# Kernel optimization log

Measured on AMD Instinct MI355X. Metric: run time of the kernel, lower is better.

Reference implementation:

```python
import jax, jax.numpy as jnp
import numpy as np

N, F, H, K = 8192, 128, 128, 16
E = N * 32


def _mlp(f, w1, b1, w2, b2, w3, b3):
    h = jax.nn.relu(f @ w1 + b1)
    h = jax.nn.relu(h @ w2 + b2)
    return h @ w3 + b3


def _edge_conv(x, w1, b1, w2, b2, w3, b3, k):
    # dynamic kNN in feature space (includes self like torch_cluster.knn with x==y)
    sn = jnp.sum(x * x, axis=1)
    d = sn[:, None] + sn[None, :] - 2.0 * (x @ x.T)  # [N,N] squared dists
    idx = jax.lax.top_k(-d, k)[1]                    # [N,k] nearest neighbors
    xj = x[idx]                                      # [N,k,H]
    xi = jnp.broadcast_to(x[:, None, :], xj.shape)
    f = jnp.concatenate([xi, xj - xi], axis=-1)      # [N,k,2H]
    return jnp.max(_mlp(f, w1, b1, w2, b2, w3, b3), axis=1)  # max aggregation


def _gcn(x, w, b, src, dst, norm, n):
    h = x @ w
    out = jax.ops.segment_sum(norm[:, None] * h[src], dst, num_segments=n)
    return out + b


def _forward(x, edge_index, edge_weight,
             wg1, bg1, wg2, bg2, wg3, bg3,
             e1w1, e1b1, e1w2, e1b2, e1w3, e1b3,
             e2w1, e2b1, e2w2, e2b2, e2w3, e2b3,
             e3w1, e3b1, e3w2, e3b2, e3w3, e3b3):
    n = x.shape[0]
    loop = jnp.arange(n)
    src = jnp.concatenate([edge_index[0], loop])  # source j
    dst = jnp.concatenate([edge_index[1], loop])  # target i
    ew = jnp.concatenate([edge_weight, jnp.ones((n,), x.dtype)])  # self-loop weight 1
    deg = jax.ops.segment_sum(ew, dst, num_segments=n)
    dis = jnp.where(deg > 0, jax.lax.rsqrt(jnp.maximum(deg, 1e-12)), 0.0)
    norm = dis[src] * ew * dis[dst]

    n1 = jnp.tanh(_gcn(x, wg1, bg1, src, dst, norm, n))   # dropout is identity at eval
    e1 = _edge_conv(n1, e1w1, e1b1, e1w2, e1b2, e1w3, e1b3, K)
    e1_n1 = jnp.linalg.norm(e1 + n1, axis=1, keepdims=True)  # [N,1]

    n2 = jnp.tanh(_gcn(n1, wg2, bg2, src, dst, norm, n))
    e2 = _edge_conv(n2, e2w1, e2b1, e2w2, e2b2, e2w3, e2b3, K)
    e2_n2 = e2 + n2

    n3 = jnp.tanh(_gcn(n2, wg3, bg3, src, dst, norm, n))
    e3 = _edge_conv(n3, e3w1, e3b1, e3w2, e3b2, e3w3, e3b3, K)
    e3_n3 = e3 + n3

    x2 = e1_n1 * e2_n2 * e3_n3
    return jax.nn.log_softmax(x2, axis=1)


def setup_inputs() -> dict:
    key = jax.random.key(0)
    ks = jax.random.split(key, 32)
    inp = {
        'x': jax.random.normal(ks[0], (N, F), dtype=jnp.float32),
        'edge_index': jax.random.randint(ks[1], (2, E), 0, N, dtype=jnp.int64) if jax.config.jax_enable_x64 else jax.random.randint(ks[1], (2, E), 0, N).astype(jnp.int32),
        'edge_weight': jax.random.uniform(ks[2], (E,), dtype=jnp.float32),
    }
    s = 0.05
    gcn_in = [F, H, H]
    for i in range(3):
        inp[f'wg{i+1}'] = jax.random.normal(ks[3 + i], (gcn_in[i], H), dtype=jnp.float32) * s
        inp[f'bg{i+1}'] = jnp.zeros((H,), jnp.float32)
    dims = [(2 * H, 64), (64, H), (H, H)]
    kk = 6
    for c in range(1, 4):
        for j, (di, do) in enumerate(dims):
            inp[f'e{c}w{j+1}'] = jax.random.normal(ks[kk], (di, do), dtype=jnp.float32) * s
            inp[f'e{c}b{j+1}'] = jnp.zeros((do,), jnp.float32)
            kk += 1
    return inp


def reference(x, edge_index, edge_weight,
              wg1, bg1, wg2, bg2, wg3, bg3,
              e1w1, e1b1, e1w2, e1b2, e1w3, e1b3,
              e2w1, e2b1, e2w2, e2b2, e2w3, e2b3,
              e3w1, e3b1, e3w2, e3b2, e3w3, e3b3):
    return _forward(x, edge_index, edge_weight,
                    wg1, bg1, wg2, bg2, wg3, bg3,
                    e1w1, e1b1, e1w2, e1b2, e1w3, e1b3,
                    e2w1, e2b1, e2w2, e2b2, e2w3, e2b3,
                    e3w1, e3b1, e3w2, e3b2, e3w3, e3b3)
```

## Files before the change

kernel.cpp:

```cpp
#include <hip/hip_runtime.h>
#include <math.h>

#define N_ 8192
#define H_ 128
#define E_ 262144
#define K_ 16
#define SLABJ 1024
#define CHUNKJ 512

typedef __attribute__((ext_vector_type(8))) short bshort8;
typedef __attribute__((ext_vector_type(16))) float f32x16;
typedef unsigned long long u64;

__global__ void k_deg_init(float* deg) {
  int i = blockIdx.x * 256 + threadIdx.x;
  deg[i] = 1.0f;
}

__global__ void k_deg_scatter(const int* __restrict__ ei, const float* __restrict__ ew,
                              float* deg) {
  int e = blockIdx.x * 256 + threadIdx.x;
  atomicAdd(&deg[ei[E_ + e]], ew[e]);
}

__global__ void k_dis(float* deg) {
  int i = blockIdx.x * 256 + threadIdx.x;
  deg[i] = rsqrtf(deg[i]);
}

__global__ void k_hist(const int* __restrict__ ei, int* hist) {
  int e = blockIdx.x * 256 + threadIdx.x;
  atomicAdd(&hist[ei[E_ + e]], 1);
}

__global__ void k_scan(int* hist, int* rowptr) {
  __shared__ int part[256];
  __shared__ int partx[257];
  int t = threadIdx.x;
  int base = t * 32;
  int loc[32];
  int s = 0;
#pragma unroll
  for (int i = 0; i < 32; ++i) { loc[i] = s; s += hist[base + i]; }
  part[t] = s;
  __syncthreads();
  if (t == 0) {
    int r = 0;
    for (int i = 0; i < 256; ++i) { partx[i] = r; r += part[i]; }
    partx[256] = r;
  }
  __syncthreads();
  int b = partx[t];
#pragma unroll
  for (int i = 0; i < 32; ++i) {
    rowptr[base + i] = b + loc[i];
    hist[base + i] = b + loc[i];
  }
  if (t == 0) rowptr[N_] = partx[256];
}

__global__ void k_edgebuild(const int* __restrict__ ei, const float* __restrict__ ew,
                            const float* __restrict__ dis, int* cursor,
                            int* __restrict__ srcS, float* __restrict__ normS) {
  int e = blockIdx.x * 256 + threadIdx.x;
  int s = ei[e], d = ei[E_ + e];
  int pos = atomicAdd(&cursor[d], 1);
  srcS[pos] = s;
  normS[pos] = dis[s] * ew[e] * dis[d];
}

__device__ __forceinline__ unsigned short f2bf_rne(float x) {
  unsigned u = __builtin_bit_cast(unsigned, x);
  unsigned r = ((u >> 16) & 1u) + 0x7fffu;
  return (unsigned short)((u + r) >> 16);
}
__device__ __forceinline__ float bf2f(unsigned short b) {
  unsigned u = ((unsigned)b) << 16;
  return __builtin_bit_cast(float, u);
}

__global__ void k_wprepG(const float* __restrict__ w, int mode,
                         bshort8* __restrict__ outH, bshort8* __restrict__ outL) {
  int id = blockIdx.x * 256 + threadIdx.x;
  int lane = id & 63, ks = (id >> 6) & 7, nt = id >> 9;
  int n = nt * 32 + (lane & 31);
  int k0 = ks * 16 + (lane >> 5) * 8;
  bshort8 h, l;
#pragma unroll
  for (int i = 0; i < 8; ++i) {
    int k = k0 + i;
    float v;
    if (mode == 0) v = w[k * 128 + n];
    else v = (n < 64) ? (w[k * 64 + n] - w[(128 + k) * 64 + n])
                      : w[(128 + k) * 64 + (n - 64)];
    unsigned short hb = f2bf_rne(v);
    h[i] = (short)hb;
    l[i] = (short)f2bf_rne(v - bf2f(hb));
  }
  outH[id] = h;
  outL[id] = l;
}

__global__ __launch_bounds__(256, 3) void k_gemmM(const float* __restrict__ A,
                                                  const bshort8* __restrict__ wfH,
                                                  const bshort8* __restrict__ wfL,
                                                  float* __restrict__ C) {
  __shared__ short aHs[32 * 132], aLs[32 * 132];
  int t = threadIdx.x;
  int r0 = blockIdx.x * 32;
  int w = t >> 6, lane = t & 63, q = lane & 31, half = lane >> 5;

  {
    int r = t >> 3;
    int kc = (t & 7) * 16;
    const float* p = A + (r0 + r) * 128 + kc;
#pragma unroll
    for (int e4 = 0; e4 < 4; ++e4) {
      float4 v = *(const float4*)(p + e4 * 4);
      float vals[4] = {v.x, v.y, v.z, v.w};
      unsigned short hs[4], ls[4];
#pragma unroll
      for (int i = 0; i < 4; ++i) {
        hs[i] = f2bf_rne(vals[i]);
        ls[i] = f2bf_rne(vals[i] - bf2f(hs[i]));
      }
      int off = r * 132 + kc + e4 * 4;
      *(u64*)&aHs[off] = ((u64)hs[0]) | ((u64)hs[1] << 16) | ((u64)hs[2] << 32) | ((u64)hs[3] << 48);
      *(u64*)&aLs[off] = ((u64)ls[0]) | ((u64)ls[1] << 16) | ((u64)ls[2] << 32) | ((u64)ls[3] << 48);
    }
  }
  bshort8 bH[8], bL[8];
#pragma unroll
  for (int ks = 0; ks < 8; ++ks) {
    bH[ks] = wfH[(w * 8 + ks) * 64 + lane];
    bL[ks] = wfL[(w * 8 + ks) * 64 + lane];
  }
  __syncthreads();

  f32x16 accP, accQ;
#pragma unroll
  for (int r = 0; r < 16; ++r) { accP[r] = 0.f; accQ[r] = 0.f; }
#pragma unroll
  for (int ks = 0; ks < 8; ++ks) {
    int off = q * 132 + ks * 16 + half * 8;
    union { bshort8 v; u64 u[2]; } aH, aL;
    aH.u[0] = *(const u64*)&aHs[off];
    aH.u[1] = *(const u64*)&aHs[off + 4];
    aL.u[0] = *(const u64*)&aLs[off];
    aL.u[1] = *(const u64*)&aLs[off + 4];
    accQ = __builtin_amdgcn_mfma_f32_32x32x16_bf16(aL.v, bH[ks], accQ, 0, 0, 0);
    accQ = __builtin_amdgcn_mfma_f32_32x32x16_bf16(aH.v, bL[ks], accQ, 0, 0, 0);
    accP = __builtin_amdgcn_mfma_f32_32x32x16_bf16(aH.v, bH[ks], accP, 0, 0, 0);
  }
#pragma unroll
  for (int reg = 0; reg < 16; ++reg) {
    int row = (reg & 3) + 8 * (reg >> 2) + 4 * half;
    C[(r0 + row) * 128 + w * 32 + q] = accP[reg] + accQ[reg];
  }
}

__global__ __launch_bounds__(256) void k_gcn_agg(const float* __restrict__ h,
                                                 const float* __restrict__ dis,
                                                 const int* __restrict__ rowptr,
                                                 const int* __restrict__ srcS,
                                                 const float* __restrict__ normS,
                                                 const float* __restrict__ bg,
                                                 float* __restrict__ n_out,
                                                 float* __restrict__ sn) {
  __shared__ float part[4];
  int t = threadIdx.x;
  int i = blockIdx.x * 2 + (t >> 7);
  int c = t & 127;
  float di = dis[i];
  float a0 = di * di * h[i * 128 + c], a1 = 0.f, a2 = 0.f, a3 = 0.f;
  int e0 = rowptr[i], e1 = rowptr[i + 1];
  int e = e0;
  for (; e + 4 <= e1; e += 4) {
    int s0 = srcS[e], s1 = srcS[e + 1], s2 = srcS[e + 2], s3 = srcS[e + 3];
    float w0 = normS[e], w1 = normS[e + 1], w2 = normS[e + 2], w3 = normS[e + 3];
    a0 += w0 * h[s0 * 128 + c];
    a1 += w1 * h[s1 * 128 + c];
    a2 += w2 * h[s2 * 128 + c];
    a3 += w3 * h[s3 * 128 + c];
  }
  for (; e < e1; ++e) a0 += normS[e] * h[srcS[e] * 128 + c];
  float v = tanhf(a0 + a1 + a2 + a3 + bg[c]);
  n_out[i * 128 + c] = v;
  float vv = v * v;
#pragma unroll
  for (int off = 32; off; off >>= 1) vv += __shfl_down(vv, off, 64);
  if ((t & 63) == 0) part[t >> 6] = vv;
  __syncthreads();
  if ((t & 127) == 0) sn[i] = part[t >> 6] + part[(t >> 6) + 1];
}

__global__ void k_fragprep(const float* __restrict__ src, bshort8* __restrict__ hiA,
                           bshort8* __restrict__ loA) {
  int t = blockIdx.x * 256 + threadIdx.x;
  int j = t >> 4, slot = t & 15;
  const float* p = src + j * 128 + slot * 8;
  float4 f0 = *(const float4*)p;
  float4 f1 = *(const float4*)(p + 4);
  float f[8] = {f0.x, f0.y, f0.z, f0.w, f1.x, f1.y, f1.z, f1.w};
  bshort8 h, l;
#pragma unroll
  for (int i = 0; i < 8; ++i) {
    unsigned short hb = f2bf_rne(f[i]);
    h[i] = (short)hb;
    l[i] = (short)f2bf_rne(f[i] - bf2f(hb));
  }
  int ks = slot >> 1, half = slot & 1;
  int dst = ((j >> 5) * 8 + ks) * 64 + half * 32 + (j & 31);
  hiA[dst] = h;
  loA[dst] = l;
}

__device__ __forceinline__ u64 packkey(float d, int j) {
  unsigned m = __builtin_bit_cast(unsigned, d);
  m = (m & 0x80000000u) ? ~m : (m | 0x80000000u);
  return (((u64)m) << 32) | (unsigned)j;
}

__device__ __forceinline__ void ins8(u64* tk, u64 x) {
  bool c[8];
#pragma unroll
  for (int s = 0; s < 8; ++s) c[s] = x < tk[s];
#pragma unroll
  for (int s = 7; s >= 1; --s) tk[s] = c[s - 1] ? tk[s - 1] : (c[s] ? x : tk[s]);
  tk[0] = c[0] ? x : tk[0];
}

__device__ __forceinline__ void ins16(u64* tk, u64 x) {
  bool c[16];
#pragma unroll
  for (int s = 0; s < 16; ++s) c[s] = x < tk[s];
#pragma unroll
  for (int s = 15; s >= 1; --s) tk[s] = c[s - 1] ? tk[s - 1] : (c[s] ? x : tk[s]);
  tk[0] = c[0] ? x : tk[0];
}

__global__ __launch_bounds__(256, 3) void k_knnA(const bshort8* __restrict__ fragHi,
                                                 const bshort8* __restrict__ fragLo,
                                                 const float* __restrict__ sn,
                                                 u64* __restrict__ candA) {
  __shared__ float snS[CHUNKJ];
  __shared__ u64 mbuf[32 * 65];
  int t = threadIdx.x;
  int qtile = blockIdx.x, chunk = blockIdx.y;
  int wave = t >> 6, lane = t & 63;
  int q = lane & 31, half = lane >> 5;

  snS[t] = sn[chunk * CHUNKJ + t];
  snS[t + 256] = sn[chunk * CHUNKJ + t + 256];

  bshort8 bHi[8], bLo[8];
#pragma unroll
  for (int ks = 0; ks < 8; ++ks) {
    int o = (qtile * 8 + ks) * 64 + lane;
    bHi[ks] = fragHi[o];
    bLo[ks] = fragLo[o];
  }
  __syncthreads();

  u64 tk[8];
#pragma unroll
  for (int s = 0; s < 8; ++s) tk[s] = ~0ULL;

  for (int ti = 0; ti < 4; ++ti) {
    int jt = chunk * 16 + wave * 4 + ti;
    f32x16 accP, accQ;
#pragma unroll
    for (int r = 0; r < 16; ++r) { accP[r] = 0.f; accQ[r] = 0.f; }
    {
      bshort8 aH[4], aL[4];
#pragma unroll
      for (int k4 = 0; k4 < 4; ++k4) {
        int o = (jt * 8 + k4) * 64 + lane;
        aH[k4] = fragHi[o];
        aL[k4] = fragLo[o];
      }
#pragma unroll
      for (int k4 = 0; k4 < 4; ++k4) {
        accQ = __builtin_amdgcn_mfma_f32_32x32x16_bf16(aL[k4], bHi[k4], accQ, 0, 0, 0);
        accQ = __builtin_amdgcn_mfma_f32_32x32x16_bf16(aH[k4], bLo[k4], accQ, 0, 0, 0);
        accP = __builtin_amdgcn_mfma_f32_32x32x16_bf16(aH[k4], bHi[k4], accP, 0, 0, 0);
      }
    }
    {
      bshort8 aH[4], aL[4];
#pragma unroll
      for (int k4 = 0; k4 < 4; ++k4) {
        int o = (jt * 8 + 4 + k4) * 64 + lane;
        aH[k4] = fragHi[o];
        aL[k4] = fragLo[o];
      }
#pragma unroll
      for (int k4 = 0; k4 < 4; ++k4) {
        accQ = __builtin_amdgcn_mfma_f32_32x32x16_bf16(aL[k4], bHi[4 + k4], accQ, 0, 0, 0);
        accQ = __builtin_amdgcn_mfma_f32_32x32x16_bf16(aH[k4], bLo[4 + k4], accQ, 0, 0, 0);
        accP = __builtin_amdgcn_mfma_f32_32x32x16_bf16(aH[k4], bHi[4 + k4], accP, 0, 0, 0);
      }
    }

    int jbase = (wave * 4 + ti) * 32;
#pragma unroll
    for (int rp = 0; rp < 8; ++rp) {
      int r0 = rp * 2;
      int row0 = (r0 & 3) + 8 * (r0 >> 2) + 4 * half;
      float d0 = snS[jbase + row0] - 2.0f * (accP[r0] + accQ[r0]);
      float d1 = snS[jbase + row0 + 1] - 2.0f * (accP[r0 + 1] + accQ[r0 + 1]);
      u64 k0 = packkey(d0, chunk * CHUNKJ + jbase + row0);
      u64 k1 = packkey(d1, chunk * CHUNKJ + jbase + row0 + 1);
      u64 km = k0 < k1 ? k0 : k1;
      if (km < tk[7]) {
        if (k0 < tk[7]) ins8(tk, k0);
        if (k1 < tk[7]) ins8(tk, k1);
      }
    }
  }

  int g = wave * 2 + half;
  __syncthreads();
#pragma unroll
  for (int s = 0; s < 8; ++s) mbuf[q * 65 + g * 8 + s] = tk[s];
  __syncthreads();
  if (t < 32) {
    int qq = qtile * 32 + t;
    int base = t * 65;
    int h0 = 0, h1 = 0, h2 = 0, h3 = 0, h4 = 0, h5 = 0, h6 = 0, h7 = 0;
    for (int step = 0; step < 16; ++step) {
      u64 best = (h0 < 8) ? mbuf[base + h0] : ~0ULL;
      int bg = 0;
      u64 b;
      b = (h1 < 8) ? mbuf[base + 8 + h1] : ~0ULL;  if (b < best) { best = b; bg = 1; }
      b = (h2 < 8) ? mbuf[base + 16 + h2] : ~0ULL; if (b < best) { best = b; bg = 2; }
      b = (h3 < 8) ? mbuf[base + 24 + h3] : ~0ULL; if (b < best) { best = b; bg = 3; }
      b = (h4 < 8) ? mbuf[base + 32 + h4] : ~0ULL; if (b < best) { best = b; bg = 4; }
      b = (h5 < 8) ? mbuf[base + 40 + h5] : ~0ULL; if (b < best) { best = b; bg = 5; }
      b = (h6 < 8) ? mbuf[base + 48 + h6] : ~0ULL; if (b < best) { best = b; bg = 6; }
      b = (h7 < 8) ? mbuf[base + 56 + h7] : ~0ULL; if (b < best) { best = b; bg = 7; }
      candA[(chunk * 16 + step) * N_ + qq] = best;
      h0 += (bg == 0); h1 += (bg == 1); h2 += (bg == 2); h3 += (bg == 3);
      h4 += (bg == 4); h5 += (bg == 5); h6 += (bg == 6); h7 += (bg == 7);
    }
  }
}

__global__ __launch_bounds__(64) void k_tauseed(const u64* __restrict__ candA,
                                                u64* __restrict__ accept,
                                                int* __restrict__ cursor,
                                                u64* __restrict__ tauKey) {
  int q = blockIdx.x * 64 + threadIdx.x;
  int h0 = 0, h1 = 0, h2 = 0, h3 = 0;
  u64 best = 0;
  for (int step = 0; step < 16; ++step) {
    best = candA[h0 * N_ + q];
    int bg = 0;
    u64 b;
    b = candA[(16 + h1) * N_ + q]; if (b < best) { best = b; bg = 1; }
    b = candA[(32 + h2) * N_ + q]; if (b < best) { best = b; bg = 2; }
    b = candA[(48 + h3) * N_ + q]; if (b < best) { best = b; bg = 3; }
    accept[step * N_ + q] = best;
    h0 += (bg == 0); h1 += (bg == 1); h2 += (bg == 2); h3 += (bg == 3);
  }
  tauKey[q] = best;
  cursor[q] = 16;
}

__global__ __launch_bounds__(256, 3) void k_knnB(const bshort8* __restrict__ fragHi,
                                                 const bshort8* __restrict__ fragLo,
                                                 const float* __restrict__ sn,
                                                 const u64* __restrict__ tauKey,
                                                 int* __restrict__ cursor,
                                                 u64* __restrict__ accept,
                                                 u64* __restrict__ accExt) {
  __shared__ float snS[SLABJ];
  int t = threadIdx.x;
  int qtile = blockIdx.x, slab = blockIdx.y + 2;
  int wave = t >> 6, lane = t & 63;
  int q = lane & 31, half = lane >> 5;
  int qg = qtile * 32 + q;

#pragma unroll
  for (int p = 0; p < 4; ++p) snS[t + 256 * p] = sn[slab * SLABJ + t + 256 * p];

  bshort8 bHi[8], bLo[8];
#pragma unroll
  for (int ks = 0; ks < 8; ++ks) {
    int o = (qtile * 8 + ks) * 64 + lane;
    bHi[ks] = fragHi[o];
    bLo[ks] = fragLo[o];
  }
  u64 tau = tauKey[qg];
  __syncthreads();

  u64 buf[6];
  int cnt = 0;

  for (int ti = 0; ti < 8; ++ti) {
    int jt = slab * 32 + wave * 8 + ti;
    f32x16 accP, accQ;
#pragma unroll
    for (int r = 0; r < 16; ++r) { accP[r] = 0.f; accQ[r] = 0.f; }
    {
      bshort8 aH[4], aL[4];
#pragma unroll
      for (int k4 = 0; k4 < 4; ++k4) {
        int o = (jt * 8 + k4) * 64 + lane;
        aH[k4] = fragHi[o];
        aL[k4] = fragLo[o];
      }
#pragma unroll
      for (int k4 = 0; k4 < 4; ++k4) {
        accQ = __builtin_amdgcn_mfma_f32_32x32x16_bf16(aL[k4], bHi[k4], accQ, 0, 0, 0);
        accQ = __builtin_amdgcn_mfma_f32_32x32x16_bf16(aH[k4], bLo[k4], accQ, 0, 0, 0);
        accP = __builtin_amdgcn_mfma_f32_32x32x16_bf16(aH[k4], bHi[k4], accP, 0, 0, 0);
      }
    }
    {
      bshort8 aH[4], aL[4];
#pragma unroll
      for (int k4 = 0; k4 < 4; ++k4) {
        int o = (jt * 8 + 4 + k4) * 64 + lane;
        aH[k4] = fragHi[o];
        aL[k4] = fragLo[o];
      }
#pragma unroll
      for (int k4 = 0; k4 < 4; ++k4) {
        accQ = __builtin_amdgcn_mfma_f32_32x32x16_bf16(aL[k4], bHi[4 + k4], accQ, 0, 0, 0);
        accQ = __builtin_amdgcn_mfma_f32_32x32x16_bf16(aH[k4], bLo[4 + k4], accQ, 0, 0, 0);
        accP = __builtin_amdgcn_mfma_f32_32x32x16_bf16(aH[k4], bHi[4 + k4], accP, 0, 0, 0);
      }
    }

    int jbase = (wave * 8 + ti) * 32;
#pragma unroll
    for (int rp = 0; rp < 8; ++rp) {
      int r0 = rp * 2;
      int row0 = (r0 & 3) + 8 * (r0 >> 2) + 4 * half;
      float d0 = snS[jbase + row0] - 2.0f * (accP[r0] + accQ[r0]);
      float d1 = snS[jbase + row0 + 1] - 2.0f * (accP[r0 + 1] + accQ[r0 + 1]);
      u64 k0 = packkey(d0, slab * SLABJ + jbase + row0);
      u64 k1 = packkey(d1, slab * SLABJ + jbase + row0 + 1);
      if (k0 <= tau) {
        if (cnt < 6) {
#pragma unroll
          for (int s = 0; s < 6; ++s)
            if (s == cnt) buf[s] = k0;
          ++cnt;
        } else {
          int pos = atomicAdd(&cursor[qg], 1);
          if (pos < 128) accept[(size_t)pos * N_ + qg] = k0;
          else if (pos < 192) accExt[(size_t)(pos - 128) * N_ + qg] = k0;
        }
      }
      if (k1 <= tau) {
        if (cnt < 6) {
#pragma unroll
          for (int s = 0; s < 6; ++s)
            if (s == cnt) buf[s] = k1;
          ++cnt;
        } else {
          int pos = atomicAdd(&cursor[qg], 1);
          if (pos < 128) accept[(size_t)pos * N_ + qg] = k1;
          else if (pos < 192) accExt[(size_t)(pos - 128) * N_ + qg] = k1;
        }
      }
    }
  }

  if (cnt > 0) {
    int pos = atomicAdd(&cursor[qg], cnt);
#pragma unroll
    for (int s = 0; s < 6; ++s) {
      if (s < cnt) {
        int slot = pos + s;
        if (slot < 128) accept[(size_t)slot * N_ + qg] = buf[s];
        else if (slot < 192) accExt[(size_t)(slot - 128) * N_ + qg] = buf[s];
      }
    }
  }
}

__global__ __launch_bounds__(256) void k_select(const u64* __restrict__ accept,
                                                const u64* __restrict__ accExt,
                                                const int* __restrict__ cursor,
                                                int* __restrict__ idxo) {
  __shared__ u64 mb[64 * 65];
  int t = threadIdx.x;
  int ql = t >> 2;
  int j = t & 3;
  int q = blockIdx.x * 64 + ql;
  int c = cursor[q];
  if (c > 192) c = 192;
  u64 tk[16];
#pragma unroll
  for (int s = 0; s < 16; ++s) tk[s] = ~0ULL;
  for (int i = j; i < c; i += 4) {
    u64 x = (i < 128) ? accept[(size_t)i * N_ + q] : accExt[(size_t)(i - 128) * N_ + q];
    if (x < tk[15]) ins16(tk, x);
  }
#pragma unroll
  for (int s = 0; s < 16; ++s) mb[ql * 65 + j * 16 + s] = tk[s];
  __syncthreads();
  if (t < 64) {
    int qq = blockIdx.x * 64 + t;
    int base = t * 65;
    int h0 = 0, h1 = 0, h2 = 0, h3 = 0;
    for (int step = 0; step < 16; ++step) {
      u64 best = mb[base + h0];
      int bg = 0;
      u64 b;
      b = mb[base + 16 + h1]; if (b < best) { best = b; bg = 1; }
      b = mb[base + 32 + h2]; if (b < best) { best = b; bg = 2; }
      b = mb[base + 48 + h3]; if (b < best) { best = b; bg = 3; }
      idxo[qq * 16 + step] = (int)(unsigned)(best & 0xffffffffULL);
      h0 += (bg == 0); h1 += (bg == 1); h2 += (bg == 2); h3 += (bg == 3);
    }
  }
}

__global__ void k_wprep(const float* __restrict__ w2, const float* __restrict__ w3,
                        bshort8* __restrict__ w2fH, bshort8* __restrict__ w2fL,
                        bshort8* __restrict__ w3fH, bshort8* __restrict__ w3fL) {
  int id = blockIdx.x * 256 + threadIdx.x;
  const float* src;
  bshort8 *dH, *dL;
  int n, k0, slot;
  if (id < 1024) {
    int lane = id & 63, ks = (id >> 6) & 3, nt = id >> 8;
    n = nt * 32 + (lane & 31);
    k0 = ks * 16 + (lane >> 5) * 8;
    src = w2; dH = w2fH; dL = w2fL; slot = id;
  } else {
    int id2 = id - 1024;
    int lane = id2 & 63, ks = (id2 >> 6) & 7, nt = id2 >> 9;
    n = nt * 32 + (lane & 31);
    k0 = ks * 16 + (lane >> 5) * 8;
    src = w3; dH = w3fH; dL = w3fL; slot = id2;
  }
  bshort8 h, l;
#pragma unroll
  for (int i = 0; i < 8; ++i) {
    float v = src[(k0 + i) * 128 + n];
    unsigned short hb = f2bf_rne(v);
    h[i] = (short)hb;
    l[i] = (short)f2bf_rne(v - bf2f(hb));
  }
  dH[slot] = h;
  dL[slot] = l;
}

__global__ __launch_bounds__(256, 3) void k_mlpM(
    const float* __restrict__ ab, const int* __restrict__ idx,
    const bshort8* __restrict__ w2fH, const bshort8* __restrict__ w2fL,
    const bshort8* __restrict__ w3fH, const bshort8* __restrict__ w3fL,
    const float* __restrict__ b1g, const float* __restrict__ b2g,
    const float* __restrict__ b3g, const float* __restrict__ nadd,
    float* __restrict__ eout) {
  __shared__ short h1H[64 * 68], h1L[64 * 68];
  __shared__ short h2H[64 * 132], h2L[64 * 132];
  int t = threadIdx.x;
  int n0 = blockIdx.x * 4;
  int w = t >> 6, lane = t & 63, q = lane & 31, half = lane >> 5;

  {
    int r = t >> 2;
    int kc = (t & 3) * 16;
    int node = n0 + (r >> 4);
    int jn = idx[node * 16 + (r & 15)];
    const float* pa = ab + node * 128 + kc;
    const float* pb = ab + jn * 128 + 64 + kc;
    const float* p1 = b1g + kc;
#pragma unroll
    for (int e4 = 0; e4 < 4; ++e4) {
      float4 va = *(const float4*)(pa + e4 * 4);
      float4 vb = *(const float4*)(pb + e4 * 4);
      float4 v1 = *(const float4*)(p1 + e4 * 4);
      float vals[4] = {va.x + vb.x + v1.x, va.y + vb.y + v1.y,
                       va.z + vb.z + v1.z, va.w + vb.w + v1.w};
      unsigned short hs[4], ls[4];
#pragma unroll
      for (int i = 0; i < 4; ++i) {
        float v = fmaxf(vals[i], 0.f);
        hs[i] = f2bf_rne(v);
        ls[i] = f2bf_rne(v - bf2f(hs[i]));
      }
      int off = r * 68 + kc + e4 * 4;
      *(u64*)&h1H[off] = ((u64)hs[0]) | ((u64)hs[1] << 16) | ((u64)hs[2] << 32) | ((u64)hs[3] << 48);
      *(u64*)&h1L[off] = ((u64)ls[0]) | ((u64)ls[1] << 16) | ((u64)ls[2] << 32) | ((u64)ls[3] << 48);
    }
  }

  bshort8 c2H[4], c2L[4];
#pragma unroll
  for (int ks = 0; ks < 4; ++ks) {
    c2H[ks] = w2fH[(w * 4 + ks) * 64 + lane];
    c2L[ks] = w2fL[(w * 4 + ks) * 64 + lane];
  }
  bshort8 c3H[8], c3L[8];
#pragma unroll
  for (int ks = 0; ks < 8; ++ks) {
    c3H[ks] = w3fH[(w * 8 + ks) * 64 + lane];
    c3L[ks] = w3fL[(w * 8 + ks) * 64 + lane];
  }
  float bias2 = b2g[w * 32 + q];
  float bias3 = b3g[w * 32 + q];
  __syncthreads();

#pragma unroll
  for (int rt = 0; rt < 2; ++rt) {
    f32x16 acc;
#pragma unroll
    for (int r = 0; r < 16; ++r) acc[r] = 0.f;
#pragma unroll
    for (int ks = 0; ks < 4; ++ks) {
      int off = (rt * 32 + q) * 68 + ks * 16 + half * 8;
      union { bshort8 v; u64 u[2]; } aH, aL;
      aH.u[0] = *(const u64*)&h1H[off];
      aH.u[1] = *(const u64*)&h1H[off + 4];
      aL.u[0] = *(const u64*)&h1L[off];
      aL.u[1] = *(const u64*)&h1L[off + 4];
      acc = __builtin_amdgcn_mfma_f32_32x32x16_bf16(aL.v, c2H[ks], acc, 0, 0, 0);
      acc = __builtin_amdgcn_mfma_f32_32x32x16_bf16(aH.v, c2L[ks], acc, 0, 0, 0);
      acc = __builtin_amdgcn_mfma_f32_32x32x16_bf16(aH.v, c2H[ks], acc, 0, 0, 0);
    }
#pragma unroll
    for (int reg = 0; reg < 16; ++reg) {
      int row = rt * 32 + (reg & 3) + 8 * (reg >> 2) + 4 * half;
      float v = fmaxf(acc[reg] + bias2, 0.f);
      unsigned short hb = f2bf_rne(v);
      h2H[row * 132 + w * 32 + q] = (short)hb;
      h2L[row * 132 + w * 32 + q] = (short)f2bf_rne(v - bf2f(hb));
    }
  }
  __syncthreads();

#pragma unroll
  for (int rt = 0; rt < 2; ++rt) {
    f32x16 acc;
#pragma unroll
    for (int r = 0; r < 16; ++r) acc[r] = 0.f;
#pragma unroll
    for (int ks = 0; ks < 8; ++ks) {
      int off = (rt * 32 + q) * 132 + ks * 16 + half * 8;
      union { bshort8 v; u64 u[2]; } aH, aL;
      aH.u[0] = *(const u64*)&h2H[off];
      aH.u[1] = *(const u64*)&h2H[off + 4];
      aL.u[0] = *(const u64*)&h2L[off];
      aL.u[1] = *(const u64*)&h2L[off + 4];
      acc = __builtin_amdgcn_mfma_f32_32x32x16_bf16(aL.v, c3H[ks], acc, 0, 0, 0);
      acc = __builtin_amdgcn_mfma_f32_32x32x16_bf16(aH.v, c3L[ks], acc, 0, 0, 0);
      acc = __builtin_amdgcn_mfma_f32_32x32x16_bf16(aH.v, c3H[ks], acc, 0, 0, 0);
    }
    float mA = -INFINITY, mB = -INFINITY;
#pragma unroll
    for (int reg = 0; reg < 8; ++reg) mA = fmaxf(mA, acc[reg]);
#pragma unroll
    for (int reg = 8; reg < 16; ++reg) mB = fmaxf(mB, acc[reg]);
    mA = fmaxf(mA, __shfl_xor(mA, 32, 64));
    mB = fmaxf(mB, __shfl_xor(mB, 32, 64));
    int col = w * 32 + q;
    int nodeA = n0 + rt * 2, nodeB = n0 + rt * 2 + 1;
    if (half == 0) {
      float v = mA + bias3;
      if (nadd) v += nadd[nodeA * 128 + col];
      eout[nodeA * 128 + col] = v;
    } else {
      float v = mB + bias3;
      if (nadd) v += nadd[nodeB * 128 + col];
      eout[nodeB * 128 + col] = v;
    }
  }
}

__global__ void k_e1n1(const float* __restrict__ e1, const float* __restrict__ n1,
                       float* s1) {
  int t = threadIdx.x;
  int node = blockIdx.x * 4 + (t >> 6);
  int lane = t & 63;
  float v0 = e1[node * 128 + lane] + n1[node * 128 + lane];
  float v1 = e1[node * 128 + 64 + lane] + n1[node * 128 + 64 + lane];
  float ss = v0 * v0 + v1 * v1;
#pragma unroll
  for (int off = 32; off; off >>= 1) ss += __shfl_down(ss, off, 64);
  if (lane == 0) s1[node] = sqrtf(ss);
}

__global__ void k_final(const float* __restrict__ s1, const float* __restrict__ e2n2,
                        const float* __restrict__ e3n3, float* __restrict__ out) {
  int t = threadIdx.x;
  int node = blockIdx.x * 4 + (t >> 6);
  int lane = t & 63;
  float s = s1[node];
  float z0 = s * e2n2[node * 128 + lane] * e3n3[node * 128 + lane];
  float z1 = s * e2n2[node * 128 + 64 + lane] * e3n3[node * 128 + 64 + lane];
  float m = fmaxf(z0, z1);
#pragma unroll
  for (int off = 32; off; off >>= 1) m = fmaxf(m, __shfl_xor(m, off, 64));
  float ex = expf(z0 - m) + expf(z1 - m);
#pragma unroll
  for (int off = 32; off; off >>= 1) ex += __shfl_xor(ex, off, 64);
  float lse = m + logf(ex);
  out[node * 128 + lane] = z0 - lse;
  out[node * 128 + 64 + lane] = z1 - lse;
}

extern "C" void kernel_launch(void* const* d_in, const int* in_sizes, int n_in,
                              void* d_out, int out_size, void* d_ws, size_t ws_size,
                              hipStream_t stream) {
  (void)in_sizes; (void)n_in; (void)out_size;
  const float* x  = (const float*)d_in[0];
  const int* ei   = (const int*)d_in[1];
  const float* ew = (const float*)d_in[2];
  const float* wg[3] = {(const float*)d_in[3], (const float*)d_in[5], (const float*)d_in[7]};
  const float* bg[3] = {(const float*)d_in[4], (const float*)d_in[6], (const float*)d_in[8]};
  const float* ew1[3] = {(const float*)d_in[9],  (const float*)d_in[15], (const float*)d_in[21]};
  const float* eb1[3] = {(const float*)d_in[10], (const float*)d_in[16], (const float*)d_in[22]};
  const float* ew2[3] = {(const float*)d_in[11], (const float*)d_in[17], (const float*)d_in[23]};
  const float* eb2[3] = {(const float*)d_in[12], (const float*)d_in[18], (const float*)d_in[24]};
  const float* ew3[3] = {(const float*)d_in[13], (const float*)d_in[19], (const float*)d_in[25]};
  const float* eb3[3] = {(const float*)d_in[14], (const float*)d_in[20], (const float*)d_in[26]};

  size_t small = (size_t)(22 * N_ + (N_ + 256) + N_ + 2 * E_);
  size_t need = (small + 65536 + (size_t)7 * N_ * H_) * sizeof(float);
  if (ws_size < need) return;

  float* ws  = (float*)d_ws;
  float* dis = ws;
  float* sn  = ws + N_;
  float* S1  = ws + 2 * N_;
  int* idx   = (int*)(ws + 3 * N_);
  u64* tauKey = (u64*)(ws + 19 * N_);
  int* cursor = (int*)(ws + 21 * N_);
  int* rowptr = (int*)(ws + 22 * N_);
  int* hist   = rowptr + N_ + 256;
  int* srcS   = hist + N_;
  float* normS = (float*)(srcS + E_);
  float* wfrag = normS + E_;
  bshort8* wgfH = (bshort8*)wfrag;
  bshort8* wgfL = wgfH + 4096;
  bshort8* w1fH = wgfL + 4096;
  bshort8* w1fL = w1fH + 4096;
  float* h   = wfrag + 65536;
  float* n1  = h + N_ * H_;
  float* n2  = n1 + N_ * H_;
  float* n3  = n2 + N_ * H_;
  float* E2  = n3 + N_ * H_;
  float* E1  = E2 + N_ * H_;
  float* ab  = E1 + N_ * H_;

  bshort8* fragHi = (bshort8*)h;
  bshort8* fragLo = (bshort8*)(h + N_ * H_ / 2);
  u64* candA  = (u64*)ab;
  u64* accept = (u64*)E1;
  bshort8* w2fH = (bshort8*)h;
  bshort8* w2fL = w2fH + 1024;
  bshort8* w3fH = w2fL + 1024;
  bshort8* w3fL = w3fH + 2048;

  float* nl[3] = {n1, n2, n3};
  float* spare[3] = {n2, n1, n2};
  float* nadd[3] = {nullptr, n2, n3};

  k_deg_init<<<N_ / 256, 256, 0, stream>>>(dis);
  k_deg_scatter<<<E_ / 256, 256, 0, stream>>>(ei, ew, dis);
  k_dis<<<N_ / 256, 256, 0, stream>>>(dis);
  hipMemsetAsync(hist, 0, N_ * sizeof(int), stream);
  k_hist<<<E_ / 256, 256, 0, stream>>>(ei, hist);
  k_scan<<<1, 256, 0, stream>>>(hist, rowptr);
  k_edgebuild<<<E_ / 256, 256, 0, stream>>>(ei, ew, dis, hist, srcS, normS);

  for (int l = 0; l < 3; ++l) {
    const float* inp = (l == 0) ? x : nl[l - 1];
    k_wprepG<<<8, 256, 0, stream>>>(wg[l], 0, wgfH, wgfL);
    k_gemmM<<<256, 256, 0, stream>>>(inp, wgfH, wgfL, h);
    k_gcn_agg<<<N_ / 2, 256, 0, stream>>>(h, dis, rowptr, srcS, normS, bg[l], nl[l], sn);
    k_fragprep<<<N_ * 16 / 256, 256, 0, stream>>>(nl[l], fragHi, fragLo);
    k_knnA<<<dim3(N_ / 32, 4), 256, 0, stream>>>(fragHi, fragLo, sn, candA);
    k_tauseed<<<N_ / 64, 64, 0, stream>>>(candA, accept, cursor, tauKey);
    k_knnB<<<dim3(N_ / 32, 6), 256, 0, stream>>>(fragHi, fragLo, sn, tauKey, cursor,
                                                 accept, (u64*)spare[l]);
    k_select<<<N_ / 64, 256, 0, stream>>>(accept, (u64*)spare[l], cursor, idx);
    k_wprepG<<<8, 256, 0, stream>>>(ew1[l], 1, w1fH, w1fL);
    k_wprep<<<12, 256, 0, stream>>>(ew2[l], ew3[l], w2fH, w2fL, w3fH, w3fL);
    k_gemmM<<<256, 256, 0, stream>>>(nl[l], w1fH, w1fL, ab);
    float* etgt = (l == 1) ? E2 : E1;
    k_mlpM<<<N_ / 4, 256, 0, stream>>>(ab, idx, w2fH, w2fL, w3fH, w3fL,
                                       eb1[l], eb2[l], eb3[l], nadd[l], etgt);
    if (l == 0) k_e1n1<<<N_ / 4, 256, 0, stream>>>(E1, n1, S1);
  }
  k_final<<<N_ / 4, 256, 0, stream>>>(S1, E2, E1, (float*)d_out);
}
```

Before: 842.1 us.

## Batch weight prep, reuse kNN fragments for MLP GEMM, restructure kNN candidate merge

All twelve weight matrices are now converted to bf16 hi/lo fragments in one launch before the layer loop, replacing three prep kernels per layer. The first edge-MLP GEMM reads the already-built kNN fragment buffers instead of re-splitting the fp32 activations. The kNN first pass now processes 1024-column slabs over 2 chunks and writes per-wave top-8 lists straight to global memory, and the in-block shared-memory merge moves into a wider tau-seed kernel. knnB also compares float distances against a precomputed float threshold instead of building packed keys first. The costs are more global traffic for the unmerged candidates, lower grid parallelism in knnA, and a possible change in tie handling at the threshold.

```diff
diff --git a/kernel.cpp b/kernel.cpp
--- a/kernel.cpp
+++ b/kernel.cpp
@@ -6,7 +6,6 @@
 #define E_ 262144
 #define K_ 16
 #define SLABJ 1024
-#define CHUNKJ 512
 
 typedef __attribute__((ext_vector_type(8))) short bshort8;
 typedef __attribute__((ext_vector_type(16))) float f32x16;
@@ -79,26 +78,45 @@
   return __builtin_bit_cast(float, u);
 }
 
-__global__ void k_wprepG(const float* __restrict__ w, int mode,
-                         bshort8* __restrict__ outH, bshort8* __restrict__ outL) {
+struct WP { const float* p[12]; };
+
+__global__ void k_wprepAll(WP wp, bshort8* __restrict__ wAll) {
   int id = blockIdx.x * 256 + threadIdx.x;
-  int lane = id & 63, ks = (id >> 6) & 7, nt = id >> 9;
-  int n = nt * 32 + (lane & 31);
-  int k0 = ks * 16 + (lane >> 5) * 8;
+  int layer = id / 7168;
+  int r = id - layer * 7168;
+  bshort8* base = wAll + layer * 14336;
+  const float* src;
+  bshort8 *dH, *dL;
+  int slot, kind;
+  if (r < 2048)      { kind = 0; slot = r;        src = wp.p[layer*4+0]; dH = base;         dL = base + 2048; }
+  else if (r < 4096) { kind = 1; slot = r - 2048; src = wp.p[layer*4+1]; dH = base + 4096;  dL = base + 6144; }
+  else if (r < 5120) { kind = 2; slot = r - 4096; src = wp.p[layer*4+2]; dH = base + 8192;  dL = base + 9216; }
+  else               { kind = 3; slot = r - 5120; src = wp.p[layer*4+3]; dH = base + 10240; dL = base + 12288; }
+  int lane = slot & 63;
+  int n, k0;
+  if (kind == 2) {
+    int ks = (slot >> 6) & 3, nt = slot >> 8;
+    n = nt * 32 + (lane & 31);
+    k0 = ks * 16 + (lane >> 5) * 8;
+  } else {
+    int ks = (slot >> 6) & 7, nt = slot >> 9;
+    n = nt * 32 + (lane & 31);
+    k0 = ks * 16 + (lane >> 5) * 8;
+  }
   bshort8 h, l;
 #pragma unroll
   for (int i = 0; i < 8; ++i) {
     int k = k0 + i;
     float v;
-    if (mode == 0) v = w[k * 128 + n];
-    else v = (n < 64) ? (w[k * 64 + n] - w[(128 + k) * 64 + n])
-                      : w[(128 + k) * 64 + (n - 64)];
+    if (kind == 1) v = (n < 64) ? (src[k * 64 + n] - src[(128 + k) * 64 + n])
+                                : src[(128 + k) * 64 + (n - 64)];
+    else v = src[k * 128 + n];
     unsigned short hb = f2bf_rne(v);
     h[i] = (short)hb;
     l[i] = (short)f2bf_rne(v - bf2f(hb));
   }
-  outH[id] = h;
-  outL[id] = l;
+  dH[slot] = h;
+  dL[slot] = l;
 }
 
 __global__ __launch_bounds__(256, 3) void k_gemmM(const float* __restrict__ A,
@@ -156,6 +174,38 @@
   for (int reg = 0; reg < 16; ++reg) {
     int row = (reg & 3) + 8 * (reg >> 2) + 4 * half;
     C[(r0 + row) * 128 + w * 32 + q] = accP[reg] + accQ[reg];
+  }
+}
+
+__global__ void k_gemmMF(const bshort8* __restrict__ fAH, const bshort8* __restrict__ fAL,
+                         const bshort8* __restrict__ wfH, const bshort8* __restrict__ wfL,
+                         float* __restrict__ C) {
+  int t = threadIdx.x;
+  int rt = blockIdx.x >> 1;
+  int w = (blockIdx.x & 1) * 2 + (t >> 6);
+  int lane = t & 63, q = lane & 31, half = lane >> 5;
+
+  bshort8 bH[8], bL[8], aH[8], aL[8];
+#pragma unroll
+  for (int ks = 0; ks < 8; ++ks) {
+    bH[ks] = wfH[(w * 8 + ks) * 64 + lane];
+    bL[ks] = wfL[(w * 8 + ks) * 64 + lane];
+    aH[ks] = fAH[(rt * 8 + ks) * 64 + lane];
+    aL[ks] = fAL[(rt * 8 + ks) * 64 + lane];
+  }
+  f32x16 accP, accQ;
+#pragma unroll
+  for (int r = 0; r < 16; ++r) { accP[r] = 0.f; accQ[r] = 0.f; }
+#pragma unroll
+  for (int ks = 0; ks < 8; ++ks) {
+    accQ = __builtin_amdgcn_mfma_f32_32x32x16_bf16(aL[ks], bH[ks], accQ, 0, 0, 0);
+    accQ = __builtin_amdgcn_mfma_f32_32x32x16_bf16(aH[ks], bL[ks], accQ, 0, 0, 0);
+    accP = __builtin_amdgcn_mfma_f32_32x32x16_bf16(aH[ks], bH[ks], accP, 0, 0, 0);
+  }
+#pragma unroll
+  for (int reg = 0; reg < 16; ++reg) {
+    int row = (reg & 3) + 8 * (reg >> 2) + 4 * half;
+    C[(rt * 32 + row) * 128 + w * 32 + q] = accP[reg] + accQ[reg];
   }
 }
 
@@ -221,6 +271,12 @@
   return (((u64)m) << 32) | (unsigned)j;
 }
 
+__device__ __forceinline__ float unpackd(u64 key) {
+  unsigned m = (unsigned)(key >> 32);
+  unsigned u = (m & 0x80000000u) ? (m & 0x7fffffffu) : ~m;
+  return __builtin_bit_cast(float, u);
+}
+
 __device__ __forceinline__ void ins8(u64* tk, u64 x) {
   bool c[8];
 #pragma unroll
@@ -242,16 +298,15 @@
 __global__ __launch_bounds__(256, 3) void k_knnA(const bshort8* __restrict__ fragHi,
                                                  const bshort8* __restrict__ fragLo,
                                                  const float* __restrict__ sn,
-                                                 u64* __restrict__ candA) {
-  __shared__ float snS[CHUNKJ];
-  __shared__ u64 mbuf[32 * 65];
+                                                 u64* __restrict__ candR) {
+  __shared__ float snS[SLABJ];
   int t = threadIdx.x;
   int qtile = blockIdx.x, chunk = blockIdx.y;
   int wave = t >> 6, lane = t & 63;
   int q = lane & 31, half = lane >> 5;
 
-  snS[t] = sn[chunk * CHUNKJ + t];
-  snS[t + 256] = sn[chunk * CHUNKJ + t + 256];
+#pragma unroll
+  for (int p = 0; p < 4; ++p) snS[t + 256 * p] = sn[chunk * SLABJ + t + 256 * p];
 
   bshort8 bHi[8], bLo[8];
 #pragma unroll
@@ -266,8 +321,8 @@
 #pragma unroll
   for (int s = 0; s < 8; ++s) tk[s] = ~0ULL;
 
-  for (int ti = 0; ti < 4; ++ti) {
-    int jt = chunk * 16 + wave * 4 + ti;
+  for (int ti = 0; ti < 8; ++ti) {
+    int jt = chunk * 32 + wave * 8 + ti;
     f32x16 accP, accQ;
 #pragma unroll
     for (int r = 0; r < 16; ++r) { accP[r] = 0.f; accQ[r] = 0.f; }
@@ -302,15 +357,15 @@
       }
     }
 
-    int jbase = (wave * 4 + ti) * 32;
+    int jbase = (wave * 8 + ti) * 32;
 #pragma unroll
     for (int rp = 0; rp < 8; ++rp) {
       int r0 = rp * 2;
       int row0 = (r0 & 3) + 8 * (r0 >> 2) + 4 * half;
       float d0 = snS[jbase + row0] - 2.0f * (accP[r0] + accQ[r0]);
       float d1 = snS[jbase + row0 + 1] - 2.0f * (accP[r0 + 1] + accQ[r0 + 1]);
-      u64 k0 = packkey(d0, chunk * CHUNKJ + jbase + row0);
-      u64 k1 = packkey(d1, chunk * CHUNKJ + jbase + row0 + 1);
+      u64 k0 = packkey(d0, chunk * SLABJ + jbase + row0);
+      u64 k1 = packkey(d1, chunk * SLABJ + jbase + row0 + 1);
       u64 km = k0 < k1 ? k0 : k1;
       if (km < tk[7]) {
         if (k0 < tk[7]) ins8(tk, k0);
@@ -320,57 +375,64 @@
   }
 
   int g = wave * 2 + half;
-  __syncthreads();
-#pragma unroll
-  for (int s = 0; s < 8; ++s) mbuf[q * 65 + g * 8 + s] = tk[s];
-  __syncthreads();
-  if (t < 32) {
-    int qq = qtile * 32 + t;
+#pragma unroll
+  for (int s = 0; s < 8; ++s)
+    candR[(size_t)(chunk * 64 + g * 8 + s) * N_ + qtile * 32 + q] = tk[s];
+}
+
+__global__ __launch_bounds__(256) void k_tauseedX(const u64* __restrict__ candR,
+                                                  u64* __restrict__ accept,
+                                                  int* __restrict__ cursor,
+                                                  u64* __restrict__ tauKey,
+                                                  float* __restrict__ tauD) {
+  __shared__ u64 mb[64 * 65];
+  int t = threadIdx.x;
+  int ql = t >> 2, j = t & 3;
+  int q = blockIdx.x * 64 + ql;
+
+  int rb[4];
+#pragma unroll
+  for (int k = 0; k < 4; ++k) {
+    int L = 4 * j + k;
+    rb[k] = (L >> 3) * 64 + (L & 7) * 8;
+  }
+  int h0 = 0, h1 = 0, h2 = 0, h3 = 0;
+  for (int step = 0; step < 16; ++step) {
+    u64 best = (h0 < 8) ? candR[(size_t)(rb[0] + h0) * N_ + q] : ~0ULL;
+    int bg = 0;
+    u64 b;
+    b = (h1 < 8) ? candR[(size_t)(rb[1] + h1) * N_ + q] : ~0ULL; if (b < best) { best = b; bg = 1; }
+    b = (h2 < 8) ? candR[(size_t)(rb[2] + h2) * N_ + q] : ~0ULL; if (b < best) { best = b; bg = 2; }
+    b = (h3 < 8) ? candR[(size_t)(rb[3] + h3) * N_ + q] : ~0ULL; if (b < best) { best = b; bg = 3; }
+    mb[ql * 65 + j * 16 + step] = best;
+    h0 += (bg == 0); h1 += (bg == 1); h2 += (bg == 2); h3 += (bg == 3);
+  }
+  __syncthreads();
+  if (t < 64) {
+    int qq = blockIdx.x * 64 + t;
     int base = t * 65;
-    int h0 = 0, h1 = 0, h2 = 0, h3 = 0, h4 = 0, h5 = 0, h6 = 0, h7 = 0;
+    int g0 = 0, g1 = 0, g2 = 0, g3 = 0;
+    u64 best = 0;
     for (int step = 0; step < 16; ++step) {
-      u64 best = (h0 < 8) ? mbuf[base + h0] : ~0ULL;
+      best = mb[base + g0];
       int bg = 0;
       u64 b;
-      b = (h1 < 8) ? mbuf[base + 8 + h1] : ~0ULL;  if (b < best) { best = b; bg = 1; }
-      b = (h2 < 8) ? mbuf[base + 16 + h2] : ~0ULL; if (b < best) { best = b; bg = 2; }
-      b = (h3 < 8) ? mbuf[base + 24 + h3] : ~0ULL; if (b < best) { best = b; bg = 3; }
-      b = (h4 < 8) ? mbuf[base + 32 + h4] : ~0ULL; if (b < best) { best = b; bg = 4; }
-      b = (h5 < 8) ? mbuf[base + 40 + h5] : ~0ULL; if (b < best) { best = b; bg = 5; }
-      b = (h6 < 8) ? mbuf[base + 48 + h6] : ~0ULL; if (b < best) { best = b; bg = 6; }
-      b = (h7 < 8) ? mbuf[base + 56 + h7] : ~0ULL; if (b < best) { best = b; bg = 7; }
-      candA[(chunk * 16 + step) * N_ + qq] = best;
-      h0 += (bg == 0); h1 += (bg == 1); h2 += (bg == 2); h3 += (bg == 3);
-      h4 += (bg == 4); h5 += (bg == 5); h6 += (bg == 6); h7 += (bg == 7);
-    }
-  }
-}
-
-__global__ __launch_bounds__(64) void k_tauseed(const u64* __restrict__ candA,
-                                                u64* __restrict__ accept,
-                                                int* __restrict__ cursor,
-                                                u64* __restrict__ tauKey) {
-  int q = blockIdx.x * 64 + threadIdx.x;
-  int h0 = 0, h1 = 0, h2 = 0, h3 = 0;
-  u64 best = 0;
-  for (int step = 0; step < 16; ++step) {
-    best = candA[h0 * N_ + q];
-    int bg = 0;
-    u64 b;
-    b = candA[(16 + h1) * N_ + q]; if (b < best) { best = b; bg = 1; }
-    b = candA[(32 + h2) * N_ + q]; if (b < best) { best = b; bg = 2; }
-    b = candA[(48 + h3) * N_ + q]; if (b < best) { best = b; bg = 3; }
-    accept[step * N_ + q] = best;
-    h0 += (bg == 0); h1 += (bg == 1); h2 += (bg == 2); h3 += (bg == 3);
-  }
-  tauKey[q] = best;
-  cursor[q] = 16;
+      b = mb[base + 16 + g1]; if (b < best) { best = b; bg = 1; }
+      b = mb[base + 32 + g2]; if (b < best) { best = b; bg = 2; }
+      b = mb[base + 48 + g3]; if (b < best) { best = b; bg = 3; }
+      accept[(size_t)step * N_ + qq] = best;
+      g0 += (bg == 0); g1 += (bg == 1); g2 += (bg == 2); g3 += (bg == 3);
+    }
+    tauKey[qq] = best;
+    tauD[qq] = unpackd(best);
+    cursor[qq] = 16;
+  }
 }
 
 __global__ __launch_bounds__(256, 3) void k_knnB(const bshort8* __restrict__ fragHi,
                                                  const bshort8* __restrict__ fragLo,
                                                  const float* __restrict__ sn,
-                                                 const u64* __restrict__ tauKey,
+                                                 const float* __restrict__ tauD,
                                                  int* __restrict__ cursor,
                                                  u64* __restrict__ accept,
                                                  u64* __restrict__ accExt) {
@@ -391,7 +453,7 @@
     bHi[ks] = fragHi[o];
     bLo[ks] = fragLo[o];
   }
-  u64 tau = tauKey[qg];
+  float tD = tauD[qg];
   __syncthreads();
 
   u64 buf[6];
@@ -440,9 +502,8 @@
       int row0 = (r0 & 3) + 8 * (r0 >> 2) + 4 * half;
       float d0 = snS[jbase + row0] - 2.0f * (accP[r0] + accQ[r0]);
       float d1 = snS[jbase + row0 + 1] - 2.0f * (accP[r0 + 1] + accQ[r0 + 1]);
-      u64 k0 = packkey(d0, slab * SLABJ + jbase + row0);
-      u64 k1 = packkey(d1, slab * SLABJ + jbase + row0 + 1);
-      if (k0 <= tau) {
+      if (d0 <= tD) {
+        u64 k0 = packkey(d0, slab * SLABJ + jbase + row0);
         if (cnt < 6) {
 #pragma unroll
           for (int s = 0; s < 6; ++s)
@@ -454,7 +515,8 @@
           else if (pos < 192) accExt[(size_t)(pos - 128) * N_ + qg] = k0;
         }
       }
-      if (k1 <= tau) {
+      if (d1 <= tD) {
+        u64 k1 = packkey(d1, slab * SLABJ + jbase + row0 + 1);
         if (cnt < 6) {
 #pragma unroll
           for (int s = 0; s < 6; ++s)
@@ -518,37 +580,6 @@
       h0 += (bg == 0); h1 += (bg == 1); h2 += (bg == 2); h3 += (bg == 3);
     }
   }
-}
-
-__global__ void k_wprep(const float* __restrict__ w2, const float* __restrict__ w3,
-                        bshort8* __restrict__ w2fH, bshort8* __restrict__ w2fL,
-                        bshort8* __restrict__ w3fH, bshort8* __restrict__ w3fL) {
-  int id = blockIdx.x * 256 + threadIdx.x;
-  const float* src;
-  bshort8 *dH, *dL;
-  int n, k0, slot;
-  if (id < 1024) {
-    int lane = id & 63, ks = (id >> 6) & 3, nt = id >> 8;
-    n = nt * 32 + (lane & 31);
-    k0 = ks * 16 + (lane >> 5) * 8;
-    src = w2; dH = w2fH; dL = w2fL; slot = id;
-  } else {
-    int id2 = id - 1024;
-    int lane = id2 & 63, ks = (id2 >> 6) & 7, nt = id2 >> 9;
-    n = nt * 32 + (lane & 31);
-    k0 = ks * 16 + (lane >> 5) * 8;
-    src = w3; dH = w3fH; dL = w3fL; slot = id2;
-  }
-  bshort8 h, l;
-#pragma unroll
-  for (int i = 0; i < 8; ++i) {
-    float v = src[(k0 + i) * 128 + n];
-    unsigned short hb = f2bf_rne(v);
-    h[i] = (short)hb;
-    l[i] = (short)f2bf_rne(v - bf2f(hb));
-  }
-  dH[slot] = h;
-  dL[slot] = l;
 }
 
 __global__ __launch_bounds__(256, 3) void k_mlpM(
@@ -722,8 +753,8 @@
   const float* ew3[3] = {(const float*)d_in[13], (const float*)d_in[19], (const float*)d_in[25]};
   const float* eb3[3] = {(const float*)d_in[14], (const float*)d_in[20], (const float*)d_in[26]};
 
-  size_t small = (size_t)(22 * N_ + (N_ + 256) + N_ + 2 * E_);
-  size_t need = (small + 65536 + (size_t)7 * N_ * H_) * sizeof(float);
+  size_t small = (size_t)(23 * N_ + (N_ + 256) + N_ + 2 * E_);
+  size_t need = (small + 172032 + (size_t)7 * N_ * H_) * sizeof(float);
   if (ws_size < need) return;
 
   float* ws  = (float*)d_ws;
@@ -733,16 +764,13 @@
   int* idx   = (int*)(ws + 3 * N_);
   u64* tauKey = (u64*)(ws + 19 * N_);
   int* cursor = (int*)(ws + 21 * N_);
-  int* rowptr = (int*)(ws + 22 * N_);
+  float* tauD = ws + 22 * N_;
+  int* rowptr = (int*)(ws + 23 * N_);
   int* hist   = rowptr + N_ + 256;
   int* srcS   = hist + N_;
   float* normS = (float*)(srcS + E_);
-  float* wfrag = normS + E_;
-  bshort8* wgfH = (bshort8*)wfrag;
-  bshort8* wgfL = wgfH + 4096;
-  bshort8* w1fH = wgfL + 4096;
-  bshort8* w1fL = w1fH + 4096;
-  float* h   = wfrag + 65536;
+  bshort8* wAll = (bshort8*)(normS + E_);
+  float* h   = (float*)(normS + E_ + 172032);
   float* n1  = h + N_ * H_;
   float* n2  = n1 + N_ * H_;
   float* n3  = n2 + N_ * H_;
@@ -752,12 +780,8 @@
 
   bshort8* fragHi = (bshort8*)h;
   bshort8* fragLo = (bshort8*)(h + N_ * H_ / 2);
-  u64* candA  = (u64*)ab;
+  u64* candR  = (u64*)E1;
   u64* accept = (u64*)E1;
-  bshort8* w2fH = (bshort8*)h;
-  bshort8* w2fL = w2fH + 1024;
-  bshort8* w3fH = w2fL + 1024;
-  bshort8* w3fL = w3fH + 2048;
 
   float* nl[3] = {n1, n2, n3};
   float* spare[3] = {n2, n1, n2};
@@ -771,20 +795,32 @@
   k_scan<<<1, 256, 0, stream>>>(hist, rowptr);
   k_edgebuild<<<E_ / 256, 256, 0, stream>>>(ei, ew, dis, hist, srcS, normS);
 
+  WP wp;
   for (int l = 0; l < 3; ++l) {
+    wp.p[l * 4 + 0] = wg[l];
+    wp.p[l * 4 + 1] = ew1[l];
+    wp.p[l * 4 + 2] = ew2[l];
+    wp.p[l * 4 + 3] = ew3[l];
+  }
+  k_wprepAll<<<84, 256, 0, stream>>>(wp, wAll);
+
+  for (int l = 0; l < 3; ++l) {
+    bshort8* wl = wAll + l * 14336;
+    bshort8* wgfH = wl;            bshort8* wgfL = wl + 2048;
+    bshort8* w1fH = wl + 4096;     bshort8* w1fL = wl + 6144;
+    bshort8* w2fH = wl + 8192;     bshort8* w2fL = wl + 9216;
+    bshort8* w3fH = wl + 10240;    bshort8* w3fL = wl + 12288;
+
     const float* inp = (l == 0) ? x : nl[l - 1];
-    k_wprepG<<<8, 256, 0, stream>>>(wg[l], 0, wgfH, wgfL);
     k_gemmM<<<256, 256, 0, stream>>>(inp, wgfH, wgfL, h);
     k_gcn_agg<<<N_ / 2, 256, 0, stream>>>(h, dis, rowptr, srcS, normS, bg[l], nl[l], sn);
     k_fragprep<<<N_ * 16 / 256, 256, 0, stream>>>(nl[l], fragHi, fragLo);
-    k_knnA<<<dim3(N_ / 32, 4), 256, 0, stream>>>(fragHi, fragLo, sn, candA);
-    k_tauseed<<<N_ / 64, 64, 0, stream>>>(candA, accept, cursor, tauKey);
-    k_knnB<<<dim3(N_ / 32, 6), 256, 0, stream>>>(fragHi, fragLo, sn, tauKey, cursor,
+    k_knnA<<<dim3(N_ / 32, 2), 256, 0, stream>>>(fragHi, fragLo, sn, candR);
+    k_tauseedX<<<N_ / 64, 256, 0, stream>>>(candR, accept, cursor, tauKey, tauD);
+    k_knnB<<<dim3(N_ / 32, 6), 256, 0, stream>>>(fragHi, fragLo, sn, tauD, cursor,
                                                  accept, (u64*)spare[l]);
     k_select<<<N_ / 64, 256, 0, stream>>>(accept, (u64*)spare[l], cursor, idx);
-    k_wprepG<<<8, 256, 0, stream>>>(ew1[l], 1, w1fH, w1fL);
-    k_wprep<<<12, 256, 0, stream>>>(ew2[l], ew3[l], w2fH, w2fL, w3fH, w3fL);
-    k_gemmM<<<256, 256, 0, stream>>>(nl[l], w1fH, w1fL, ab);
+    k_gemmMF<<<512, 128, 0, stream>>>(fragHi, fragLo, w1fH, w1fL, ab);
     float* etgt = (l == 1) ? E2 : E1;
     k_mlpM<<<N_ / 4, 256, 0, stream>>>(ab, idx, w2fH, w2fL, w3fH, w3fL,
                                        eb1[l], eb2[l], eb3[l], nadd[l], etgt);
```

New measurement: 817.6 us. 2.9% less time.
